# Kernel optimization log

Hardware: AMD Instinct MI355X
Metric: run time of the kernel (lower is better)

## Reference

```python
import jax, jax.numpy as jnp
import numpy as np

NMS_THR = 0.5
PULL_W = 1.0
PUSH_W = 1.0
EPS = 1e-6


def _pairwise_iou(b1, b2):
    # mmdet-style IoU with the +1 pixel convention. b1: [M,4], b2: [N,4] -> [M,N]
    lt = jnp.maximum(b1[:, None, :2], b2[None, :, :2])
    rb = jnp.minimum(b1[:, None, 2:], b2[None, :, 2:])
    wh = jnp.clip(rb - lt + 1.0, 0.0)
    overlap = wh[..., 0] * wh[..., 1]
    a1 = (b1[:, 2] - b1[:, 0] + 1.0) * (b1[:, 3] - b1[:, 1] + 1.0)
    a2 = (b2[:, 2] - b2[:, 0] + 1.0) * (b2[:, 3] - b2[:, 1] + 1.0)
    return overlap / (a1[:, None] + a2[None, :] - overlap)


def _single_img(gt_inds, gt_box, props):
    # gt_inds: [N] int32 (>=0 positive, <0 ignore), gt_box: [G,4], props: [N,5]
    N = props.shape[0]
    G = gt_box.shape[0]
    pos = gt_inds >= 0
    boxes = props[:, :4]
    scores = props[:, 4]
    # push_select=True: rows of the IoU matrix are detached, columns carry grad
    iou = _pairwise_iou(jax.lax.stop_gradient(boxes), boxes)
    gt_iou = _pairwise_iou(gt_box, gt_box)
    safe_g = jnp.maximum(gt_inds, 0)
    score_key = jax.lax.stop_gradient(scores)
    NEG = jnp.float32(-1e30)

    def step(carry, _):
        alive, rec, tpull, tpush, pcnt, qcnt = carry
        any_alive = jnp.any(alive)
        i = jnp.argmax(jnp.where(alive, score_key, NEG))  # pop highest score
        g = safe_g[i]
        alive_p = alive.at[i].set(False)
        # pull: toward the recorded max-score box of the same gt
        has_rec = rec[g] >= 0
        rec_i = jnp.maximum(rec[g], 0)
        ms_iou = jnp.maximum(iou[i, rec_i], EPS)
        pull = -jnp.log(ms_iou) * scores[i]  # pull_relax=False, use_score=True
        # push: overlapping survivors assigned to a different gt, whose IoU
        # with i exceeds the gt-gt IoU
        row = iou[i]
        overlap = alive_p & (row > NMS_THR)
        final = overlap & (gt_inds != g) & (row > gt_iou[g, safe_g])
        cnt = jnp.sum(final)
        safe_row = jnp.where(final, row, 0.0)
        lj = -jnp.log(1.0 + NMS_THR - safe_row) * score_key  # push_relax=True, score detached
        push = jnp.where(cnt > 0,
                         jnp.sum(jnp.where(final, lj, 0.0)) / jnp.maximum(cnt, 1).astype(row.dtype),
                         0.0)
        remaining = jnp.any(alive_p)
        add = any_alive & remaining  # torch breaks BEFORE accumulating when idx empties
        tpull = tpull + jnp.where(add & has_rec, pull, 0.0)
        tpush = tpush + jnp.where(add, push, 0.0)
        pcnt = pcnt + jnp.where(any_alive & has_rec, 1, 0)  # counted even on the break step
        qcnt = qcnt + jnp.where(add, cnt, 0)
        new_rec = jnp.where(any_alive & ~has_rec, rec.at[g].set(i.astype(jnp.int32)), rec)
        new_alive = jnp.where(any_alive, alive_p & ~overlap, alive)
        return (new_alive, new_rec, tpull, tpush, pcnt, qcnt), None

    init = (pos, jnp.full((G,), -1, jnp.int32), jnp.float32(0.0), jnp.float32(0.0),
            jnp.int32(0), jnp.int32(0))
    (alive, rec, tpull, tpush, pcnt, qcnt), _ = jax.lax.scan(step, init, None, length=N)
    valid = (jnp.sum(pos) > 1).astype(jnp.float32)  # <=1 positive -> zero loss
    pull_loss = tpull / (pcnt.astype(jnp.float32) + EPS) * valid
    push_loss = tpush / (qcnt.astype(jnp.float32) + EPS) * valid
    return push_loss, pull_loss


def _make_boxes(key, shape):
    xy = jax.random.uniform(key, shape[:-1] + (2,)) * 800.0
    wh = jax.random.uniform(jax.random.fold_in(key, 1), shape[:-1] + (2,)) * 200.0 + 8.0
    return jnp.concatenate([xy, xy + wh], axis=-1)


def setup_inputs() -> dict:
    key = jax.random.key(0)
    B, N, G = 4, 2048, 64
    k0, k1, k2, k3 = jax.random.split(key, 4)
    boxes = _make_boxes(k0, (B, N, 4))
    scores = jax.random.uniform(k1, (B, N, 1))
    proposal_list = jnp.concatenate([boxes, scores], axis=-1)
    gt_bboxes = _make_boxes(k2, (B, G, 4))
    anchor_gt_inds = jax.random.randint(k3, (B, N), 0, G, dtype=jnp.int32)
    return {
        "gt_inds": anchor_gt_inds,  # ignored: single_nms_loss overwrites it
        "anchor_gt_inds": anchor_gt_inds,
        "gt_bboxes": gt_bboxes,
        "proposal_list": proposal_list,
    }


def reference(gt_inds, anchor_gt_inds, gt_bboxes, proposal_list):
    push, pull = jax.vmap(_single_img)(anchor_gt_inds, gt_bboxes, proposal_list)
    push_loss = jnp.mean(push) * PUSH_W
    pull_loss = jnp.mean(pull) * PULL_W
    return jnp.stack([push_loss, pull_loss])  # [nms_push_loss, nms_pull_loss]
```

## Files before the change

kernel.cpp:

```cpp
#include <hip/hip_runtime.h>

#define NN 2048
#define GG 64
#define TS 128
#define NT (NN / TS)
#define NPAIR (NT * (NT + 1) / 2)
#define MAXE 14336
#define EBUF 3072
#define STH 512

typedef unsigned long long u64;
typedef unsigned short u16;
typedef unsigned int u32;

__device__ __forceinline__ float iou4(float4 a, float4 b) {
    float w = fminf(a.z, b.z) - fmaxf(a.x, b.x) + 1.0f;
    float h = fminf(a.w, b.w) - fmaxf(a.y, b.y) + 1.0f;
    w = fmaxf(w, 0.0f);
    h = fmaxf(h, 0.0f);
    float ov = w * h;
    float aa = (a.z - a.x + 1.0f) * (a.w - a.y + 1.0f);
    float ab = (b.z - b.x + 1.0f) * (b.w - b.y + 1.0f);
    return ov / (aa + ab - ov);
}

__device__ __forceinline__ float wredf(float v) {
    for (int o = 32; o > 0; o >>= 1) v += __shfl_down(v, o);
    return v;
}
__device__ __forceinline__ int wredi(int v) {
    for (int o = 32; o > 0; o >>= 1) v += __shfl_down(v, o);
    return v;
}
__device__ __forceinline__ u64 wredmin64(u64 v) {
    for (int o = 32; o > 0; o >>= 1) {
        u64 w = __shfl_down(v, o);
        v = (w < v) ? w : v;
    }
    return v;
}

__device__ __forceinline__ bool earlier(u32 sa, int a, u32 sb, int b) {
    return (sa > sb) || (sa == sb && a < b);
}
__device__ __forceinline__ u64 make_key(u32 sbits, int j) {
    return ((u64)sbits << 32) | (u64)(NN - 1 - j);
}
__device__ __forceinline__ float4 load_box(const float* pb, int j) {
    return make_float4(pb[j * 5 + 0], pb[j * 5 + 1], pb[j * 5 + 2], pb[j * 5 + 3]);
}

__global__ __launch_bounds__(256) void pair_kernel(const int* __restrict__ gt_inds,
                                                   const float* __restrict__ props,
                                                   int* __restrict__ ecnt, u32* __restrict__ edges) {
    const int im = blockIdx.x / NPAIR;
    int q = blockIdx.x % NPAIR;
    int ta = 0;
    while (q >= NT - ta) { q -= NT - ta; ++ta; }
    const int tb = ta + q;
    const float* pb = props + (size_t)im * NN * 5;
    const int* gbi = gt_inds + (size_t)im * NN;

    __shared__ float4 Abox[TS], Bbox[TS];
    __shared__ u32 Asc[TS], Bsc[TS];
    __shared__ int Ag[TS], Bg[TS];
    __shared__ u32 ebuf[EBUF];
    __shared__ int lcnt, gbase;
    const int tid = threadIdx.x;
    if (tid == 0) lcnt = 0;

    for (int t = tid; t < 2 * TS; t += 256) {
        int half = t >> 7, r = t & (TS - 1);
        int j = (half ? tb : ta) * TS + r;
        float4 bx = load_box(pb, j);
        u32 sb = __float_as_uint(pb[j * 5 + 4]);
        int g = gbi[j];
        if (half == 0) { Abox[r] = bx; Asc[r] = sb; Ag[r] = g; }
        else           { Bbox[r] = bx; Bsc[r] = sb; Bg[r] = g; }
    }
    __syncthreads();

    const int pr = tid & (TS - 1);
    const int half = tid >> 7;
    const float4 rb = Abox[pr];
    const u32 rs = Asc[pr];
    const int i = ta * TS + pr;
    int* ec = ecnt + im * 32;
    u32* ge = edges + (size_t)im * MAXE;
    if (Ag[pr] >= 0) {
        #pragma unroll 4
        for (int k = 0; k < TS / 2; ++k) {
            int jl = half * (TS / 2) + k;
            if (ta == tb && jl <= pr) continue;
            if (Bg[jl] < 0) continue;
            float v = iou4(rb, Bbox[jl]);
            if (v > 0.5f) {
                int j = tb * TS + jl;
                int late, early;
                if (earlier(rs, i, Bsc[jl], j)) { late = j; early = i; }
                else                            { late = i; early = j; }
                u32 packed = ((u32)late << 16) | (u32)early;
                int slot = atomicAdd(&lcnt, 1);
                if (slot < EBUF) ebuf[slot] = packed;
                else {
                    int gs = atomicAdd(ec, 1);
                    if (gs < MAXE) ge[gs] = packed;
                }
            }
        }
    }
    __syncthreads();
    const int n = min(lcnt, EBUF);
    if (tid == 0) gbase = (n > 0) ? atomicAdd(ec, n) : 0;
    __syncthreads();
    for (int e = tid; e < n; e += 256) {
        int gidx = gbase + e;
        if (gidx < MAXE) ge[gidx] = ebuf[e];
    }
}

union SumWl {
    float sumA[NN];
    u16 wl[2][NN];
};

__global__ __launch_bounds__(STH) void scan_kernel(const int* __restrict__ gt_inds,
                                                   const float* __restrict__ gt_boxes,
                                                   const float* __restrict__ props,
                                                   const int* __restrict__ ecnt, const u32* __restrict__ edges,
                                                   float* __restrict__ acc, u32* __restrict__ ctr2,
                                                   float* __restrict__ out, int B) {
    __shared__ u32 scoreL[NN];
    __shared__ SumWl u;
    __shared__ int cw[NN];
    __shared__ u16 eoff[NN + 1];
    __shared__ u16 ent[MAXE];
    __shared__ unsigned char st[NN];
    __shared__ unsigned char hk[NN];
    __shared__ float4 gtb[GG];
    __shared__ u64 firstk[GG];
    __shared__ int wtot[STH / 64];
    __shared__ int s_cnt[2];
    __shared__ u64 s_minkey;
    __shared__ int s_pos, s_qcnt, s_pcnt;
    __shared__ float s_tpush, s_tpull;

    const int im = blockIdx.x, tid = threadIdx.x;
    const int lane = tid & 63, wid = tid >> 6;
    const float* pb = props + (size_t)im * NN * 5;
    const int* gbi = gt_inds + (size_t)im * NN;
    const u32* ge = edges + (size_t)im * MAXE;
    volatile unsigned char* vst = st;

    if (tid == 0) {
        s_pos = 0; s_qcnt = 0; s_pcnt = 0; s_tpush = 0.f; s_tpull = 0.f; s_minkey = ~0ull;
        s_cnt[0] = 0; s_cnt[1] = 0;
    }
    if (tid < GG) {
        firstk[tid] = 0ull;
        const float* gt = gt_boxes + (size_t)im * GG * 4;
        gtb[tid] = make_float4(gt[tid * 4 + 0], gt[tid * 4 + 1], gt[tid * 4 + 2], gt[tid * 4 + 3]);
    }
    int lpos = 0;
    for (int j = tid; j < NN; j += STH) {
        int g = gbi[j];
        st[j] = (g >= 0) ? 0 : 2;
        lpos += (g >= 0) ? 1 : 0;
        scoreL[j] = __float_as_uint(pb[j * 5 + 4]);
        cw[j] = 0; hk[j] = 0;
    }
    lpos = wredi(lpos);
    if (lane == 0 && lpos) atomicAdd(&s_pos, lpos);
    __syncthreads();

    const int E = min(ecnt[im * 32], MAXE);
    for (int e = tid; e < E; e += STH) atomicAdd(&cw[ge[e] >> 16], 1);
    __syncthreads();
    {
        int j0 = tid * 4;
        int c0 = cw[j0], c1 = cw[j0 + 1], c2 = cw[j0 + 2], c3 = cw[j0 + 3];
        int s = c0 + c1 + c2 + c3;
        int incl = s;
        for (int o = 1; o < 64; o <<= 1) {
            int v = __shfl_up(incl, o);
            if (lane >= o) incl += v;
        }
        if (lane == 63) wtot[wid] = incl;
        __syncthreads();
        int wpre = 0;
        for (int wq = 0; wq < wid; ++wq) wpre += wtot[wq];
        int excl = wpre + incl - s;
        eoff[j0] = (u16)excl;
        eoff[j0 + 1] = (u16)(excl + c0);
        eoff[j0 + 2] = (u16)(excl + c0 + c1);
        eoff[j0 + 3] = (u16)(excl + c0 + c1 + c2);
        if (tid == STH - 1) eoff[NN] = (u16)(excl + s);
        cw[j0] = excl;
        cw[j0 + 1] = excl + c0;
        cw[j0 + 2] = excl + c0 + c1;
        cw[j0 + 3] = excl + c0 + c1 + c2;
    }
    __syncthreads();
    for (int e = tid; e < E; e += STH) {
        u32 x = ge[e];
        int pos = atomicAdd(&cw[x >> 16], 1);
        ent[pos] = (u16)(x & 0xffffu);
    }
    __syncthreads();

    for (int j = tid; j < NN; j += STH) {
        if (st[j] != 0) continue;
        int e0 = eoff[j], e1 = eoff[j + 1];
        bool anyK = false, anyU = false;
        for (int e = e0; e < e1; ++e) {
            unsigned char s = vst[ent[e]];
            anyK |= (s == 1);
            anyU |= (s == 0);
        }
        if (anyK) st[j] = 2;
        else if (!anyU) st[j] = 1;
        else { int pos = atomicAdd(&s_cnt[0], 1); u.wl[0][pos] = (u16)j; }
    }
    __syncthreads();

    int src = 0;
    int nwl = s_cnt[0];
    while (nwl > 0) {
        #pragma unroll
        for (int r = 0; r < 2; ++r) {
            for (int w = tid; w < nwl; w += STH) {
                int j = u.wl[src][w];
                if (st[j] != 0) continue;
                int e0 = eoff[j], e1 = eoff[j + 1];
                bool anyK = false, anyU = false;
                for (int e = e0; e < e1; ++e) {
                    unsigned char s = vst[ent[e]];
                    anyK |= (s == 1);
                    anyU |= (s == 0);
                }
                if (anyK) st[j] = 2;
                else if (!anyU) st[j] = 1;
            }
        }
        for (int w = tid; w < nwl; w += STH) {
            int j = u.wl[src][w];
            if (st[j] != 0) continue;
            int e0 = eoff[j], e1 = eoff[j + 1];
            bool anyK = false, anyU = false;
            for (int e = e0; e < e1; ++e) {
                unsigned char s = vst[ent[e]];
                anyK |= (s == 1);
                anyU |= (s == 0);
            }
            if (anyK) st[j] = 2;
            else if (!anyU) st[j] = 1;
            else { int pos = atomicAdd(&s_cnt[src ^ 1], 1); u.wl[src ^ 1][pos] = (u16)j; }
        }
        __syncthreads();
        nwl = s_cnt[src ^ 1];
        if (tid == 0) s_cnt[src] = 0;
        src ^= 1;
        __syncthreads();
    }

    for (int j = tid; j < NN; j += STH) { u.sumA[j] = 0.f; cw[j] = 0; }
    __syncthreads();

    u64 lmin = ~0ull;
    for (int j = tid; j < NN; j += STH) {
        if (st[j] != 1) continue;
        u64 kj = make_key(scoreL[j], j);
        if (kj < lmin) lmin = kj;
        atomicMax(&firstk[gbi[j]], kj);
    }
    lmin = wredmin64(lmin);
    if (lane == 0 && lmin != ~0ull) atomicMin(&s_minkey, lmin);

    for (int j = tid; j < NN; j += STH) {
        int g = gbi[j];
        if (st[j] != 2 || g < 0) continue;
        int e0 = eoff[j], e1 = eoff[j + 1];
        int ki = -1; u32 ks = 0;
        for (int e = e0; e < e1; ++e) {
            int ii = ent[e];
            if (st[ii] == 1 && (ki < 0 || earlier(scoreL[ii], ii, ks, ki))) { ki = ii; ks = scoreL[ii]; }
        }
        if (ki < 0) continue;
        hk[ki] = 1;
        float v = iou4(load_box(pb, ki), load_box(pb, j));
        int gi = gbi[ki];
        if (g != gi && v > iou4(gtb[gi], gtb[g])) {
            atomicAdd(&cw[ki], 1);
            atomicAdd(&u.sumA[ki], -logf(1.5f - v) * pb[j * 5 + 4]);
        }
    }
    __syncthreads();

    float ltpush = 0.f, ltpull = 0.f;
    int lqcnt = 0, lpcnt = 0;
    const u64 minkey = s_minkey;
    for (int i = tid; i < NN; i += STH) {
        if (st[i] != 1) continue;
        int g = gbi[i];
        u64 ky = make_key(scoreL[i], i);
        u64 fk = firstk[g];
        bool add = (ky != minkey) || (hk[i] != 0);
        int c = cw[i];
        bool hr = fk > ky;
        if (add && c > 0) ltpush += u.sumA[i] / (float)c;
        if (add) lqcnt += c;
        if (hr) ++lpcnt;
        if (add && hr) {
            int r = (NN - 1) - (int)(fk & 0xffffffffu);
            float v = iou4(load_box(pb, i), load_box(pb, r));
            ltpull += -logf(fmaxf(v, 1e-6f)) * pb[i * 5 + 4];
        }
    }
    ltpush = wredf(ltpush); ltpull = wredf(ltpull);
    lqcnt = wredi(lqcnt); lpcnt = wredi(lpcnt);
    if (lane == 0) {
        if (ltpush != 0.f) atomicAdd(&s_tpush, ltpush);
        if (ltpull != 0.f) atomicAdd(&s_tpull, ltpull);
        if (lqcnt) atomicAdd(&s_qcnt, lqcnt);
        if (lpcnt) atomicAdd(&s_pcnt, lpcnt);
    }
    __syncthreads();

    if (tid == 0) {
        float valid = (s_pos > 1) ? 1.0f : 0.0f;
        float push_b = s_tpush / ((float)s_qcnt + 1e-6f) * valid;
        float pull_b = s_tpull / ((float)s_pcnt + 1e-6f) * valid;
        atomicAdd(&acc[0], push_b);
        atomicAdd(&acc[1], pull_b);
        __threadfence();
        u32 old = atomicAdd(ctr2, 1u);
        if (old == (u32)(B - 1)) {
            float ps = atomicAdd(&acc[0], 0.0f);
            float pl = atomicAdd(&acc[1], 0.0f);
            float inv = 1.0f / (float)B;
            out[0] = ps * inv * 1.0f;
            out[1] = pl * inv * 1.0f;
        }
    }
}

extern "C" void kernel_launch(void* const* d_in, const int* in_sizes, int n_in,
                              void* d_out, int out_size, void* d_ws, size_t ws_size,
                              hipStream_t stream) {
    const int B = in_sizes[0] / NN;
    const int* anchor_gt = (const int*)d_in[1];
    const float* gtb = (const float*)d_in[2];
    const float* props = (const float*)d_in[3];

    char* w = (char*)d_ws;
    int* ecnt = (int*)w;
    float* acc = (float*)(w + (size_t)B * 128);
    u32* ctr2 = (u32*)(w + (size_t)B * 128 + 8);
    size_t hdr = ((size_t)B * 128 + 12 + 127) & ~(size_t)127;
    u32* edges = (u32*)(w + hdr);

    hipMemsetAsync(d_ws, 0, hdr, stream);
    pair_kernel<<<dim3(B * NPAIR), dim3(256), 0, stream>>>(anchor_gt, props, ecnt, edges);
    scan_kernel<<<dim3(B), dim3(STH), 0, stream>>>(anchor_gt, gtb, props, ecnt, edges,
                                                   acc, ctr2, (float*)d_out, B);
}
```

Before: 54.93 us.

## Repack proposals into SoA workspace, replace memset with init kernel, widen scan block

Adds an init kernel that stages each image's AoS proposals through shared memory into separate float4 box, score and gt-index arrays in workspace. It also zeroes the counters, replacing the memset. Pair and scan kernels then read boxes with aligned vector loads, and the scan kernel caches each gt's recorded box in shared memory. The scan block grows from 512 to 1024 threads to shorten its serial loops, at the cost of an extra kernel launch and more synchronisation per block.

New measurement: 48.33 us. 12.0% less time.

```diff
diff --git a/kernel.cpp b/kernel.cpp
--- a/kernel.cpp
+++ b/kernel.cpp
@@ -7,7 +7,7 @@
 #define NPAIR (NT * (NT + 1) / 2)
 #define MAXE 14336
 #define EBUF 3072
-#define STH 512
+#define STH 1024
 
 typedef unsigned long long u64;
 typedef unsigned short u16;
@@ -46,20 +46,40 @@
 __device__ __forceinline__ u64 make_key(u32 sbits, int j) {
     return ((u64)sbits << 32) | (u64)(NN - 1 - j);
 }
-__device__ __forceinline__ float4 load_box(const float* pb, int j) {
-    return make_float4(pb[j * 5 + 0], pb[j * 5 + 1], pb[j * 5 + 2], pb[j * 5 + 3]);
-}
-
-__global__ __launch_bounds__(256) void pair_kernel(const int* __restrict__ gt_inds,
+
+__global__ __launch_bounds__(256) void init_kernel(const int* __restrict__ gt_inds,
                                                    const float* __restrict__ props,
+                                                   float4* __restrict__ sbox, float* __restrict__ ssc,
+                                                   int* __restrict__ sgt,
+                                                   int* __restrict__ ecnt, float* __restrict__ acc,
+                                                   u32* __restrict__ ctr2) {
+    __shared__ float pbL[NN * 5];
+    const int im = blockIdx.x, tid = threadIdx.x;
+    if (tid < 32) ecnt[im * 32 + tid] = 0;
+    if (im == 0 && tid == 0) { acc[0] = 0.f; acc[1] = 0.f; *ctr2 = 0u; }
+    const float4* pv = (const float4*)(props + (size_t)im * NN * 5);
+    float4* pl4 = (float4*)pbL;
+    for (int x = tid; x < NN * 5 / 4; x += 256) pl4[x] = pv[x];
+    __syncthreads();
+    const int base = im * NN;
+    const int* gbi = gt_inds + (size_t)im * NN;
+    for (int j = tid; j < NN; j += 256) {
+        sbox[base + j] = make_float4(pbL[j * 5], pbL[j * 5 + 1], pbL[j * 5 + 2], pbL[j * 5 + 3]);
+        ssc[base + j] = pbL[j * 5 + 4];
+        sgt[base + j] = gbi[j];
+    }
+}
+
+__global__ __launch_bounds__(256) void pair_kernel(const float4* __restrict__ sbox,
+                                                   const float* __restrict__ ssc,
+                                                   const int* __restrict__ sgt,
                                                    int* __restrict__ ecnt, u32* __restrict__ edges) {
     const int im = blockIdx.x / NPAIR;
     int q = blockIdx.x % NPAIR;
     int ta = 0;
     while (q >= NT - ta) { q -= NT - ta; ++ta; }
     const int tb = ta + q;
-    const float* pb = props + (size_t)im * NN * 5;
-    const int* gbi = gt_inds + (size_t)im * NN;
+    const int base = im * NN;
 
     __shared__ float4 Abox[TS], Bbox[TS];
     __shared__ u32 Asc[TS], Bsc[TS];
@@ -69,14 +89,13 @@
     const int tid = threadIdx.x;
     if (tid == 0) lcnt = 0;
 
-    for (int t = tid; t < 2 * TS; t += 256) {
-        int half = t >> 7, r = t & (TS - 1);
-        int j = (half ? tb : ta) * TS + r;
-        float4 bx = load_box(pb, j);
-        u32 sb = __float_as_uint(pb[j * 5 + 4]);
-        int g = gbi[j];
-        if (half == 0) { Abox[r] = bx; Asc[r] = sb; Ag[r] = g; }
-        else           { Bbox[r] = bx; Bsc[r] = sb; Bg[r] = g; }
+    for (int t = tid; t < TS; t += 256) {
+        Abox[t] = sbox[base + ta * TS + t];
+        Asc[t] = __float_as_uint(ssc[base + ta * TS + t]);
+        Ag[t] = sgt[base + ta * TS + t];
+        Bbox[t] = sbox[base + tb * TS + t];
+        Bsc[t] = __float_as_uint(ssc[base + tb * TS + t]);
+        Bg[t] = sgt[base + tb * TS + t];
     }
     __syncthreads();
 
@@ -124,20 +143,22 @@
     u16 wl[2][NN];
 };
 
-__global__ __launch_bounds__(STH) void scan_kernel(const int* __restrict__ gt_inds,
+__global__ __launch_bounds__(STH) void scan_kernel(const int* __restrict__ sgt,
                                                    const float* __restrict__ gt_boxes,
-                                                   const float* __restrict__ props,
+                                                   const float4* __restrict__ sbox,
+                                                   const float* __restrict__ ssc,
                                                    const int* __restrict__ ecnt, const u32* __restrict__ edges,
                                                    float* __restrict__ acc, u32* __restrict__ ctr2,
                                                    float* __restrict__ out, int B) {
     __shared__ u32 scoreL[NN];
     __shared__ SumWl u;
     __shared__ int cw[NN];
-    __shared__ u16 eoff[NN + 1];
+    __shared__ u16 eoff[NN + 2];
     __shared__ u16 ent[MAXE];
     __shared__ unsigned char st[NN];
     __shared__ unsigned char hk[NN];
     __shared__ float4 gtb[GG];
+    __shared__ float4 recbox[GG];
     __shared__ u64 firstk[GG];
     __shared__ int wtot[STH / 64];
     __shared__ int s_cnt[2];
@@ -147,8 +168,7 @@
 
     const int im = blockIdx.x, tid = threadIdx.x;
     const int lane = tid & 63, wid = tid >> 6;
-    const float* pb = props + (size_t)im * NN * 5;
-    const int* gbi = gt_inds + (size_t)im * NN;
+    const int base = im * NN;
     const u32* ge = edges + (size_t)im * MAXE;
     volatile unsigned char* vst = st;
 
@@ -158,15 +178,14 @@
     }
     if (tid < GG) {
         firstk[tid] = 0ull;
-        const float* gt = gt_boxes + (size_t)im * GG * 4;
-        gtb[tid] = make_float4(gt[tid * 4 + 0], gt[tid * 4 + 1], gt[tid * 4 + 2], gt[tid * 4 + 3]);
+        gtb[tid] = ((const float4*)(gt_boxes + (size_t)im * GG * 4))[tid];
     }
     int lpos = 0;
     for (int j = tid; j < NN; j += STH) {
-        int g = gbi[j];
+        int g = sgt[base + j];
         st[j] = (g >= 0) ? 0 : 2;
         lpos += (g >= 0) ? 1 : 0;
-        scoreL[j] = __float_as_uint(pb[j * 5 + 4]);
+        scoreL[j] = __float_as_uint(ssc[base + j]);
         cw[j] = 0; hk[j] = 0;
     }
     lpos = wredi(lpos);
@@ -177,9 +196,9 @@
     for (int e = tid; e < E; e += STH) atomicAdd(&cw[ge[e] >> 16], 1);
     __syncthreads();
     {
-        int j0 = tid * 4;
-        int c0 = cw[j0], c1 = cw[j0 + 1], c2 = cw[j0 + 2], c3 = cw[j0 + 3];
-        int s = c0 + c1 + c2 + c3;
+        int j0 = tid * 2;
+        int c0 = cw[j0], c1 = cw[j0 + 1];
+        int s = c0 + c1;
         int incl = s;
         for (int o = 1; o < 64; o <<= 1) {
             int v = __shfl_up(incl, o);
@@ -192,13 +211,9 @@
         int excl = wpre + incl - s;
         eoff[j0] = (u16)excl;
         eoff[j0 + 1] = (u16)(excl + c0);
-        eoff[j0 + 2] = (u16)(excl + c0 + c1);
-        eoff[j0 + 3] = (u16)(excl + c0 + c1 + c2);
         if (tid == STH - 1) eoff[NN] = (u16)(excl + s);
         cw[j0] = excl;
         cw[j0 + 1] = excl + c0;
-        cw[j0 + 2] = excl + c0 + c1;
-        cw[j0 + 3] = excl + c0 + c1 + c2;
     }
     __syncthreads();
     for (int e = tid; e < E; e += STH) {
@@ -271,13 +286,19 @@
         if (st[j] != 1) continue;
         u64 kj = make_key(scoreL[j], j);
         if (kj < lmin) lmin = kj;
-        atomicMax(&firstk[gbi[j]], kj);
+        atomicMax(&firstk[sgt[base + j]], kj);
     }
     lmin = wredmin64(lmin);
     if (lane == 0 && lmin != ~0ull) atomicMin(&s_minkey, lmin);
+    __syncthreads();
+
+    if (tid < GG) {
+        u64 fk = firstk[tid];
+        if (fk) recbox[tid] = sbox[base + (NN - 1) - (int)(fk & 0xffffffffu)];
+    }
 
     for (int j = tid; j < NN; j += STH) {
-        int g = gbi[j];
+        int g = sgt[base + j];
         if (st[j] != 2 || g < 0) continue;
         int e0 = eoff[j], e1 = eoff[j + 1];
         int ki = -1; u32 ks = 0;
@@ -287,11 +308,11 @@
         }
         if (ki < 0) continue;
         hk[ki] = 1;
-        float v = iou4(load_box(pb, ki), load_box(pb, j));
-        int gi = gbi[ki];
+        float v = iou4(sbox[base + ki], sbox[base + j]);
+        int gi = sgt[base + ki];
         if (g != gi && v > iou4(gtb[gi], gtb[g])) {
             atomicAdd(&cw[ki], 1);
-            atomicAdd(&u.sumA[ki], -logf(1.5f - v) * pb[j * 5 + 4]);
+            atomicAdd(&u.sumA[ki], -logf(1.5f - v) * __uint_as_float(scoreL[j]));
         }
     }
     __syncthreads();
@@ -301,7 +322,7 @@
     const u64 minkey = s_minkey;
     for (int i = tid; i < NN; i += STH) {
         if (st[i] != 1) continue;
-        int g = gbi[i];
+        int g = sgt[base + i];
         u64 ky = make_key(scoreL[i], i);
         u64 fk = firstk[g];
         bool add = (ky != minkey) || (hk[i] != 0);
@@ -311,9 +332,8 @@
         if (add) lqcnt += c;
         if (hr) ++lpcnt;
         if (add && hr) {
-            int r = (NN - 1) - (int)(fk & 0xffffffffu);
-            float v = iou4(load_box(pb, i), load_box(pb, r));
-            ltpull += -logf(fmaxf(v, 1e-6f)) * pb[i * 5 + 4];
+            float v = iou4(sbox[base + i], recbox[g]);
+            ltpull += -logf(fmaxf(v, 1e-6f)) * __uint_as_float(scoreL[i]);
         }
     }
     ltpush = wredf(ltpush); ltpull = wredf(ltpull);
@@ -356,11 +376,14 @@
     int* ecnt = (int*)w;
     float* acc = (float*)(w + (size_t)B * 128);
     u32* ctr2 = (u32*)(w + (size_t)B * 128 + 8);
-    size_t hdr = ((size_t)B * 128 + 12 + 127) & ~(size_t)127;
-    u32* edges = (u32*)(w + hdr);
-
-    hipMemsetAsync(d_ws, 0, hdr, stream);
-    pair_kernel<<<dim3(B * NPAIR), dim3(256), 0, stream>>>(anchor_gt, props, ecnt, edges);
-    scan_kernel<<<dim3(B), dim3(STH), 0, stream>>>(anchor_gt, gtb, props, ecnt, edges,
+    size_t o = (size_t)B * 128 + 128;
+    float4* sbox = (float4*)(w + o);   o += (size_t)B * NN * 16;
+    float* ssc = (float*)(w + o);      o += (size_t)B * NN * 4;
+    int* sgt = (int*)(w + o);          o += (size_t)B * NN * 4;
+    u32* edges = (u32*)(w + o);
+
+    init_kernel<<<dim3(B), dim3(256), 0, stream>>>(anchor_gt, props, sbox, ssc, sgt, ecnt, acc, ctr2);
+    pair_kernel<<<dim3(B * NPAIR), dim3(256), 0, stream>>>(sbox, ssc, sgt, ecnt, edges);
+    scan_kernel<<<dim3(B), dim3(STH), 0, stream>>>(sgt, gtb, sbox, ssc, ecnt, edges,
                                                    acc, ctr2, (float*)d_out, B);
 }
```

## Use per-block edge slots, drop memset, cache boxes in LDS, double scan threads

Applied to the files above, without the earlier changes.

The pair kernel now writes each tile-pair's edges into its own fixed-capacity slot in global memory and records a per-block count. This replaces the global atomic append and lets the hipMemsetAsync launch be removed, since acc and ctr2 are now zeroed by block 0. The scan kernel doubles its thread count to 1024, caches all proposal boxes and gt indices in shared memory, and precomputes the boxes recorded per gt, so later phases read LDS instead of global memory. The risks are heavier shared-memory use and occupancy, silent truncation of any tile pair with more than CAPBLK edges, and a race between block 0 zeroing acc and the scan kernel, which is only safe because of stream ordering.

New measurement: 48.77 us. -11.2%, faster.

```diff
diff --git a/kernel.cpp b/kernel.cpp
--- a/kernel.cpp
+++ b/kernel.cpp
@@ -6,8 +6,9 @@
 #define NT (NN / TS)
 #define NPAIR (NT * (NT + 1) / 2)
 #define MAXE 14336
-#define EBUF 3072
-#define STH 512
+#define CAPBLK 2048
+#define STH 1024
+#define NWAVE (STH / 64)
 
 typedef unsigned long long u64;
 typedef unsigned short u16;
@@ -52,9 +53,11 @@
 
 __global__ __launch_bounds__(256) void pair_kernel(const int* __restrict__ gt_inds,
                                                    const float* __restrict__ props,
-                                                   int* __restrict__ ecnt, u32* __restrict__ edges) {
+                                                   int* __restrict__ counts, u32* __restrict__ edges,
+                                                   float* __restrict__ acc, u32* __restrict__ ctr2) {
     const int im = blockIdx.x / NPAIR;
-    int q = blockIdx.x % NPAIR;
+    const int p = blockIdx.x % NPAIR;
+    int q = p;
     int ta = 0;
     while (q >= NT - ta) { q -= NT - ta; ++ta; }
     const int tb = ta + q;
@@ -64,19 +67,20 @@
     __shared__ float4 Abox[TS], Bbox[TS];
     __shared__ u32 Asc[TS], Bsc[TS];
     __shared__ int Ag[TS], Bg[TS];
-    __shared__ u32 ebuf[EBUF];
-    __shared__ int lcnt, gbase;
+    __shared__ u32 ebuf[CAPBLK];
+    __shared__ int lcnt;
     const int tid = threadIdx.x;
     if (tid == 0) lcnt = 0;
+    if (blockIdx.x == 0 && tid == 0) { acc[0] = 0.f; acc[1] = 0.f; *ctr2 = 0u; }
 
     for (int t = tid; t < 2 * TS; t += 256) {
         int half = t >> 7, r = t & (TS - 1);
         int j = (half ? tb : ta) * TS + r;
-        float4 bx = load_box(pb, j);
+        float4 bxv = load_box(pb, j);
         u32 sb = __float_as_uint(pb[j * 5 + 4]);
         int g = gbi[j];
-        if (half == 0) { Abox[r] = bx; Asc[r] = sb; Ag[r] = g; }
-        else           { Bbox[r] = bx; Bsc[r] = sb; Bg[r] = g; }
+        if (half == 0) { Abox[r] = bxv; Asc[r] = sb; Ag[r] = g; }
+        else           { Bbox[r] = bxv; Bsc[r] = sb; Bg[r] = g; }
     }
     __syncthreads();
 
@@ -85,8 +89,6 @@
     const float4 rb = Abox[pr];
     const u32 rs = Asc[pr];
     const int i = ta * TS + pr;
-    int* ec = ecnt + im * 32;
-    u32* ge = edges + (size_t)im * MAXE;
     if (Ag[pr] >= 0) {
         #pragma unroll 4
         for (int k = 0; k < TS / 2; ++k) {
@@ -99,24 +101,16 @@
                 int late, early;
                 if (earlier(rs, i, Bsc[jl], j)) { late = j; early = i; }
                 else                            { late = i; early = j; }
-                u32 packed = ((u32)late << 16) | (u32)early;
                 int slot = atomicAdd(&lcnt, 1);
-                if (slot < EBUF) ebuf[slot] = packed;
-                else {
-                    int gs = atomicAdd(ec, 1);
-                    if (gs < MAXE) ge[gs] = packed;
-                }
+                if (slot < CAPBLK) ebuf[slot] = ((u32)late << 16) | (u32)early;
             }
         }
     }
     __syncthreads();
-    const int n = min(lcnt, EBUF);
-    if (tid == 0) gbase = (n > 0) ? atomicAdd(ec, n) : 0;
-    __syncthreads();
-    for (int e = tid; e < n; e += 256) {
-        int gidx = gbase + e;
-        if (gidx < MAXE) ge[gidx] = ebuf[e];
-    }
+    const int n = min(lcnt, CAPBLK);
+    if (tid == 0) counts[blockIdx.x] = n;
+    u32* ge = edges + (size_t)blockIdx.x * CAPBLK;
+    for (int e = tid; e < n; e += 256) ge[e] = ebuf[e];
 }
 
 union SumWl {
@@ -127,19 +121,23 @@
 __global__ __launch_bounds__(STH) void scan_kernel(const int* __restrict__ gt_inds,
                                                    const float* __restrict__ gt_boxes,
                                                    const float* __restrict__ props,
-                                                   const int* __restrict__ ecnt, const u32* __restrict__ edges,
+                                                   const int* __restrict__ counts, const u32* __restrict__ edges,
                                                    float* __restrict__ acc, u32* __restrict__ ctr2,
                                                    float* __restrict__ out, int B) {
+    __shared__ float4 bx[NN];
     __shared__ u32 scoreL[NN];
     __shared__ SumWl u;
     __shared__ int cw[NN];
-    __shared__ u16 eoff[NN + 1];
+    __shared__ u16 eoff[NN + 2];
     __shared__ u16 ent[MAXE];
     __shared__ unsigned char st[NN];
     __shared__ unsigned char hk[NN];
+    __shared__ signed char gtL[NN];
+    __shared__ int rcnt[NPAIR];
     __shared__ float4 gtb[GG];
+    __shared__ float4 recbox[GG];
     __shared__ u64 firstk[GG];
-    __shared__ int wtot[STH / 64];
+    __shared__ int wtot[NWAVE];
     __shared__ int s_cnt[2];
     __shared__ u64 s_minkey;
     __shared__ int s_pos, s_qcnt, s_pcnt;
@@ -149,7 +147,6 @@
     const int lane = tid & 63, wid = tid >> 6;
     const float* pb = props + (size_t)im * NN * 5;
     const int* gbi = gt_inds + (size_t)im * NN;
-    const u32* ge = edges + (size_t)im * MAXE;
     volatile unsigned char* vst = st;
 
     if (tid == 0) {
@@ -158,28 +155,34 @@
     }
     if (tid < GG) {
         firstk[tid] = 0ull;
-        const float* gt = gt_boxes + (size_t)im * GG * 4;
-        gtb[tid] = make_float4(gt[tid * 4 + 0], gt[tid * 4 + 1], gt[tid * 4 + 2], gt[tid * 4 + 3]);
-    }
+        gtb[tid] = ((const float4*)(gt_boxes + (size_t)im * GG * 4))[tid];
+    }
+    if (tid < NPAIR) rcnt[tid] = counts[im * NPAIR + tid];
+
     int lpos = 0;
     for (int j = tid; j < NN; j += STH) {
+        bx[j] = load_box(pb, j);
+        scoreL[j] = __float_as_uint(pb[j * 5 + 4]);
         int g = gbi[j];
+        gtL[j] = (signed char)((g < 0) ? -1 : g);
         st[j] = (g >= 0) ? 0 : 2;
         lpos += (g >= 0) ? 1 : 0;
-        scoreL[j] = __float_as_uint(pb[j * 5 + 4]);
         cw[j] = 0; hk[j] = 0;
     }
     lpos = wredi(lpos);
     if (lane == 0 && lpos) atomicAdd(&s_pos, lpos);
     __syncthreads();
 
-    const int E = min(ecnt[im * 32], MAXE);
-    for (int e = tid; e < E; e += STH) atomicAdd(&cw[ge[e] >> 16], 1);
+    for (int r = wid; r < NPAIR; r += NWAVE) {
+        int cr = rcnt[r];
+        const u32* ge = edges + (size_t)(im * NPAIR + r) * CAPBLK;
+        for (int e = lane; e < cr; e += 64) atomicAdd(&cw[ge[e] >> 16], 1);
+    }
     __syncthreads();
     {
-        int j0 = tid * 4;
-        int c0 = cw[j0], c1 = cw[j0 + 1], c2 = cw[j0 + 2], c3 = cw[j0 + 3];
-        int s = c0 + c1 + c2 + c3;
+        int j0 = tid * 2;
+        int c0 = cw[j0], c1 = cw[j0 + 1];
+        int s = c0 + c1;
         int incl = s;
         for (int o = 1; o < 64; o <<= 1) {
             int v = __shfl_up(incl, o);
@@ -192,19 +195,19 @@
         int excl = wpre + incl - s;
         eoff[j0] = (u16)excl;
         eoff[j0 + 1] = (u16)(excl + c0);
-        eoff[j0 + 2] = (u16)(excl + c0 + c1);
-        eoff[j0 + 3] = (u16)(excl + c0 + c1 + c2);
         if (tid == STH - 1) eoff[NN] = (u16)(excl + s);
         cw[j0] = excl;
         cw[j0 + 1] = excl + c0;
-        cw[j0 + 2] = excl + c0 + c1;
-        cw[j0 + 3] = excl + c0 + c1 + c2;
-    }
-    __syncthreads();
-    for (int e = tid; e < E; e += STH) {
-        u32 x = ge[e];
-        int pos = atomicAdd(&cw[x >> 16], 1);
-        ent[pos] = (u16)(x & 0xffffu);
+    }
+    __syncthreads();
+    for (int r = wid; r < NPAIR; r += NWAVE) {
+        int cr = rcnt[r];
+        const u32* ge = edges + (size_t)(im * NPAIR + r) * CAPBLK;
+        for (int e = lane; e < cr; e += 64) {
+            u32 x = ge[e];
+            int pos = atomicAdd(&cw[x >> 16], 1);
+            ent[pos] = (u16)(x & 0xffffu);
+        }
     }
     __syncthreads();
 
@@ -271,13 +274,19 @@
         if (st[j] != 1) continue;
         u64 kj = make_key(scoreL[j], j);
         if (kj < lmin) lmin = kj;
-        atomicMax(&firstk[gbi[j]], kj);
+        atomicMax(&firstk[gtL[j]], kj);
     }
     lmin = wredmin64(lmin);
     if (lane == 0 && lmin != ~0ull) atomicMin(&s_minkey, lmin);
+    __syncthreads();
+
+    if (tid < GG) {
+        u64 fk = firstk[tid];
+        if (fk) recbox[tid] = bx[(NN - 1) - (int)(fk & 0xffffffffu)];
+    }
 
     for (int j = tid; j < NN; j += STH) {
-        int g = gbi[j];
+        int g = gtL[j];
         if (st[j] != 2 || g < 0) continue;
         int e0 = eoff[j], e1 = eoff[j + 1];
         int ki = -1; u32 ks = 0;
@@ -287,11 +296,11 @@
         }
         if (ki < 0) continue;
         hk[ki] = 1;
-        float v = iou4(load_box(pb, ki), load_box(pb, j));
-        int gi = gbi[ki];
+        float v = iou4(bx[ki], bx[j]);
+        int gi = gtL[ki];
         if (g != gi && v > iou4(gtb[gi], gtb[g])) {
             atomicAdd(&cw[ki], 1);
-            atomicAdd(&u.sumA[ki], -logf(1.5f - v) * pb[j * 5 + 4]);
+            atomicAdd(&u.sumA[ki], -logf(1.5f - v) * __uint_as_float(scoreL[j]));
         }
     }
     __syncthreads();
@@ -301,7 +310,7 @@
     const u64 minkey = s_minkey;
     for (int i = tid; i < NN; i += STH) {
         if (st[i] != 1) continue;
-        int g = gbi[i];
+        int g = gtL[i];
         u64 ky = make_key(scoreL[i], i);
         u64 fk = firstk[g];
         bool add = (ky != minkey) || (hk[i] != 0);
@@ -311,9 +320,8 @@
         if (add) lqcnt += c;
         if (hr) ++lpcnt;
         if (add && hr) {
-            int r = (NN - 1) - (int)(fk & 0xffffffffu);
-            float v = iou4(load_box(pb, i), load_box(pb, r));
-            ltpull += -logf(fmaxf(v, 1e-6f)) * pb[i * 5 + 4];
+            float v = iou4(bx[i], recbox[g]);
+            ltpull += -logf(fmaxf(v, 1e-6f)) * __uint_as_float(scoreL[i]);
         }
     }
     ltpush = wredf(ltpush); ltpull = wredf(ltpull);
@@ -353,14 +361,13 @@
     const float* props = (const float*)d_in[3];
 
     char* w = (char*)d_ws;
-    int* ecnt = (int*)w;
-    float* acc = (float*)(w + (size_t)B * 128);
-    u32* ctr2 = (u32*)(w + (size_t)B * 128 + 8);
-    size_t hdr = ((size_t)B * 128 + 12 + 127) & ~(size_t)127;
-    u32* edges = (u32*)(w + hdr);
-
-    hipMemsetAsync(d_ws, 0, hdr, stream);
-    pair_kernel<<<dim3(B * NPAIR), dim3(256), 0, stream>>>(anchor_gt, props, ecnt, edges);
-    scan_kernel<<<dim3(B), dim3(STH), 0, stream>>>(anchor_gt, gtb, props, ecnt, edges,
+    float* acc = (float*)w;
+    u32* ctr2 = (u32*)(w + 8);
+    int* counts = (int*)(w + 128);
+    size_t o = 128 + ((size_t)B * NPAIR * 4 + 127 & ~(size_t)127);
+    u32* edges = (u32*)(w + o);
+
+    pair_kernel<<<dim3(B * NPAIR), dim3(256), 0, stream>>>(anchor_gt, props, counts, edges, acc, ctr2);
+    scan_kernel<<<dim3(B), dim3(STH), 0, stream>>>(anchor_gt, gtb, props, counts, edges,
                                                    acc, ctr2, (float*)d_out, B);
 }
```
